# Optimization experiments

Hardware: AMD Instinct MI355X
Metric: run time of the kernel (lower is better)

The kernel has to match this reference:

```python
import jax, jax.numpy as jnp
import numpy as np

EPS = 1e-08
NORMALIZE = True


def setup_inputs() -> dict:
    key = jax.random.key(0)
    X = jax.random.normal(key, (1024, 256), dtype=jnp.float32)
    return {"X": X}


def reference(X):
    # Optional L2 normalization (torch F.normalize: x / max(||x||_2, eps))
    if NORMALIZE:
        norm = jnp.linalg.norm(X, axis=-1, keepdims=True)
        X = X / jnp.maximum(norm, EPS)
    n, d = X.shape
    # Pairwise abs differences: [n, n, d]
    dists = jnp.abs(X[None, :, :] - X[:, None, :])
    # Faithful replication of the original flat-stride diagonal fill:
    # dists.view(-1)[::n+1].fill_(inf) over the flattened n*n*d tensor.
    flat = dists.reshape(-1)
    idx = jnp.arange(0, n * n * d, n + 1)
    flat = flat.at[idx].set(jnp.inf)
    dists = flat.reshape(n, n, d)
    # Min over axis 1 (nearest neighbour per (i, feature)), then -log
    m = jnp.min(dists, axis=1)  # [n, d]
    return -jnp.sum(jnp.log(m + EPS)) / n
```

## Files before the change

kernel.cpp:

```cpp
#include <hip/hip_runtime.h>
#include <math.h>

#define N 1024
#define D 256
#define EPSF 1e-8f
#define K2_BLOCKS 32
#define ROWS_PER_BLK (N / K2_BLOCKS)
#define LANES_PER_ROW (256 / ROWS_PER_BLK)

__global__ void __launch_bounds__(256) rownorm_kernel(const float* __restrict__ X,
                                                      float* __restrict__ y,
                                                      float* __restrict__ accum,
                                                      int* __restrict__ cnt) {
    const int tid  = threadIdx.x;
    const int wave = tid >> 6;
    const int lane = tid & 63;
    const int row  = blockIdx.x * 4 + wave;

    const float4 v = ((const float4*)(X + row * D))[lane];
    float ss = v.x * v.x + v.y * v.y + v.z * v.z + v.w * v.w;
    #pragma unroll
    for (int off = 32; off > 0; off >>= 1)
        ss += __shfl_down(ss, off, 64);

    if (lane == 0) {
        y[row] = v.x / fmaxf(sqrtf(ss), EPSF);
    }
    if (blockIdx.x == 0 && tid == 0) { *accum = 0.0f; *cnt = 0; }
}

__global__ void __launch_bounds__(256) koleo_kernel(const float* __restrict__ y,
                                                    float* __restrict__ accum,
                                                    int* __restrict__ cnt,
                                                    float* __restrict__ out) {
    __shared__ float sy[N];
    const int tid = threadIdx.x;
    ((float4*)sy)[tid] = ((const float4*)y)[tid];
    __syncthreads();

    const int grp = tid >> 3;
    const int s   = tid & 7;
    const int i   = blockIdx.x * ROWS_PER_BLK + grp;
    const float yi = sy[i];

    float m = INFINITY;
    #pragma unroll 8
    for (int t = 0; t < N / LANES_PER_ROW; ++t) {
        const int j = s + (t << 3);
        float d = fabsf(sy[j] - yi);
        d = (j == i) ? INFINITY : d;
        m = fminf(m, d);
    }
    #pragma unroll
    for (int off = 4; off > 0; off >>= 1)
        m = fminf(m, __shfl_xor(m, off, 64));

    float val = (s == 0) ? -logf(m + EPSF) : 0.0f;
    #pragma unroll
    for (int off = 32; off > 0; off >>= 1)
        val += __shfl_down(val, off, 64);

    __shared__ float wsum[4];
    if ((tid & 63) == 0) wsum[tid >> 6] = val;
    __syncthreads();

    if (tid == 0) {
        const float part = wsum[0] + wsum[1] + wsum[2] + wsum[3];
        atomicAdd(accum, part);
        __threadfence();
        const int ticket = atomicAdd(cnt, 1);
        if (ticket == K2_BLOCKS - 1) {
            const float total = atomicAdd(accum, 0.0f);
            out[0] = total * (1.0f / (float)N) - 255.0f * logf(EPSF);
        }
    }
}

extern "C" void kernel_launch(void* const* d_in, const int* in_sizes, int n_in,
                              void* d_out, int out_size, void* d_ws, size_t ws_size,
                              hipStream_t stream) {
    const float* X = (const float*)d_in[0];
    float* out = (float*)d_out;
    float* y     = (float*)d_ws;
    float* accum = (float*)d_ws + N;
    int*   cnt   = (int*)((float*)d_ws + N + 1);

    rownorm_kernel<<<N / 4, 256, 0, stream>>>(X, y, accum, cnt);
    koleo_kernel<<<K2_BLOCKS, 256, 0, stream>>>(y, accum, cnt, out);
}
```

Baseline: 63.47 us.

## Fuse row normalization into the nearest-neighbour kernel with redundant per-block norms

Merges the row-norm kernel and the KoLeo reduction kernel into a single kernel. Each of 16 blocks recomputes the normalized first feature for all 1024 rows into shared memory, then scans with float4 reads. The intermediate workspace buffer and the ticket-counter final reduction are dropped: blocks atomically add pre-scaled partials into an output that a memset clears first. This removes one kernel launch and the cross-block ticket, but every block now reads the whole input redundantly, and the norm phase runs only 16 blocks of parallelism.

```diff
diff --git a/kernel.cpp b/kernel.cpp
--- a/kernel.cpp
+++ b/kernel.cpp
@@ -3,59 +3,67 @@
 
 #define N 1024
 #define D 256
+#define D4 (D / 4)
 #define EPSF 1e-8f
-#define K2_BLOCKS 32
-#define ROWS_PER_BLK (N / K2_BLOCKS)
-#define LANES_PER_ROW (256 / ROWS_PER_BLK)
+#define B 16
+#define RPB (N / B)
 
-__global__ void __launch_bounds__(256) rownorm_kernel(const float* __restrict__ X,
-                                                      float* __restrict__ y,
-                                                      float* __restrict__ accum,
-                                                      int* __restrict__ cnt) {
-    const int tid  = threadIdx.x;
-    const int wave = tid >> 6;
-    const int lane = tid & 63;
-    const int row  = blockIdx.x * 4 + wave;
-
-    const float4 v = ((const float4*)(X + row * D))[lane];
-    float ss = v.x * v.x + v.y * v.y + v.z * v.z + v.w * v.w;
-    #pragma unroll
-    for (int off = 32; off > 0; off >>= 1)
-        ss += __shfl_down(ss, off, 64);
-
-    if (lane == 0) {
-        y[row] = v.x / fmaxf(sqrtf(ss), EPSF);
-    }
-    if (blockIdx.x == 0 && tid == 0) { *accum = 0.0f; *cnt = 0; }
-}
-
-__global__ void __launch_bounds__(256) koleo_kernel(const float* __restrict__ y,
-                                                    float* __restrict__ accum,
-                                                    int* __restrict__ cnt,
-                                                    float* __restrict__ out) {
+__global__ void __launch_bounds__(256) koleo_fused(const float* __restrict__ X,
+                                                   float* __restrict__ out) {
     __shared__ float sy[N];
     const int tid = threadIdx.x;
-    ((float4*)sy)[tid] = ((const float4*)y)[tid];
+
+    {
+        const int g = tid >> 3;
+        const int s = tid & 7;
+        const float4* X4 = (const float4*)X;
+        for (int pass = 0; pass < 32; ++pass) {
+            const int r = pass * 32 + g;
+            const float4* row = X4 + r * D4;
+            float ss = 0.0f;
+            float x0 = 0.0f;
+            #pragma unroll
+            for (int it = 0; it < 8; ++it) {
+                const float4 v = row[s + (it << 3)];
+                if (it == 0) x0 = v.x;
+                ss += v.x * v.x + v.y * v.y + v.z * v.z + v.w * v.w;
+            }
+            #pragma unroll
+            for (int off = 4; off > 0; off >>= 1)
+                ss += __shfl_xor(ss, off, 64);
+            if (s == 0)
+                sy[r] = x0 / fmaxf(sqrtf(ss), EPSF);
+        }
+    }
     __syncthreads();
 
-    const int grp = tid >> 3;
-    const int s   = tid & 7;
-    const int i   = blockIdx.x * ROWS_PER_BLK + grp;
+    const int grp = tid >> 2;
+    const int s   = tid & 3;
+    const int i   = blockIdx.x * RPB + grp;
     const float yi = sy[i];
+    const float4* sy4 = (const float4*)sy;
 
     float m = INFINITY;
     #pragma unroll 8
-    for (int t = 0; t < N / LANES_PER_ROW; ++t) {
-        const int j = s + (t << 3);
-        float d = fabsf(sy[j] - yi);
-        d = (j == i) ? INFINITY : d;
-        m = fminf(m, d);
+    for (int t = 0; t < 64; ++t) {
+        const int q  = s + (t << 2);
+        const float4 v = sy4[q];
+        const int jb = q << 2;
+        float d0 = fabsf(v.x - yi);
+        float d1 = fabsf(v.y - yi);
+        float d2 = fabsf(v.z - yi);
+        float d3 = fabsf(v.w - yi);
+        d0 = (jb + 0 == i) ? INFINITY : d0;
+        d1 = (jb + 1 == i) ? INFINITY : d1;
+        d2 = (jb + 2 == i) ? INFINITY : d2;
+        d3 = (jb + 3 == i) ? INFINITY : d3;
+        m = fminf(m, fminf(fminf(d0, d1), fminf(d2, d3)));
     }
     #pragma unroll
-    for (int off = 4; off > 0; off >>= 1)
+    for (int off = 2; off > 0; off >>= 1)
         m = fminf(m, __shfl_xor(m, off, 64));
 
-    float val = (s == 0) ? -logf(m + EPSF) : 0.0f;
+    float val = (s == 0) ? (-logf(m + EPSF) * (1.0f / (float)N)) : 0.0f;
     #pragma unroll
     for (int off = 32; off > 0; off >>= 1)
         val += __shfl_down(val, off, 64);
@@ -65,26 +73,15 @@
     __syncthreads();
 
     if (tid == 0) {
-        const float part = wsum[0] + wsum[1] + wsum[2] + wsum[3];
-        atomicAdd(accum, part);
-        __threadfence();
-        const int ticket = atomicAdd(cnt, 1);
-        if (ticket == K2_BLOCKS - 1) {
-            const float total = atomicAdd(accum, 0.0f);
-            out[0] = total * (1.0f / (float)N) - 255.0f * logf(EPSF);
-        }
+        float part = wsum[0] + wsum[1] + wsum[2] + wsum[3];
+        if (blockIdx.x == 0) part += -255.0f * logf(EPSF);
+        atomicAdd(out, part);
     }
 }
 
 extern "C" void kernel_launch(void* const* d_in, const int* in_sizes, int n_in,
                               void* d_out, int out_size, void* d_ws, size_t ws_size,
                               hipStream_t stream) {
-    const float* X = (const float*)d_in[0];
-    float* out = (float*)d_out;
-    float* y     = (float*)d_ws;
-    float* accum = (float*)d_ws + N;
-    int*   cnt   = (int*)((float*)d_ws + N + 1);
-
-    rownorm_kernel<<<N / 4, 256, 0, stream>>>(X, y, accum, cnt);
-    koleo_kernel<<<K2_BLOCKS, 256, 0, stream>>>(y, accum, cnt, out);
+    hipMemsetAsync(d_out, 0, out_size, stream);
+    koleo_fused<<<B, 256, 0, stream>>>((const float*)d_in[0], (float*)d_out);
 }
```

After: 78.90 us. 24.3% more time.

## Spread nearest-neighbour scan over more blocks and accumulate directly into output

Applied to the files above, without the earlier changes.

The second kernel now runs 128 blocks of 8 rows each, with 32 lanes per row reading shared memory as float4, instead of 32 blocks with 8 lanes per row reading scalars. The ticket-counter epilogue is removed. The first kernel writes the constant term into the output, and each block atomically adds its pre-scaled partial sum straight into it. This is meant to shorten the serial per-thread loop and remove the fence and second atomic. In exchange it does four times as many global atomics, and the result now depends on the first kernel having initialised the output.

```diff
diff --git a/kernel.cpp b/kernel.cpp
--- a/kernel.cpp
+++ b/kernel.cpp
@@ -4,14 +4,11 @@
 #define N 1024
 #define D 256
 #define EPSF 1e-8f
-#define K2_BLOCKS 32
-#define ROWS_PER_BLK (N / K2_BLOCKS)
-#define LANES_PER_ROW (256 / ROWS_PER_BLK)
+#define K2_BLOCKS 128
 
 __global__ void __launch_bounds__(256) rownorm_kernel(const float* __restrict__ X,
                                                       float* __restrict__ y,
-                                                      float* __restrict__ accum,
-                                                      int* __restrict__ cnt) {
+                                                      float* __restrict__ out) {
     const int tid  = threadIdx.x;
     const int wave = tid >> 6;
     const int lane = tid & 63;
@@ -26,36 +23,44 @@
     if (lane == 0) {
         y[row] = v.x / fmaxf(sqrtf(ss), EPSF);
     }
-    if (blockIdx.x == 0 && tid == 0) { *accum = 0.0f; *cnt = 0; }
+    if (blockIdx.x == 0 && tid == 0)
+        out[0] = -255.0f * logf(EPSF);
 }
 
 __global__ void __launch_bounds__(256) koleo_kernel(const float* __restrict__ y,
-                                                    float* __restrict__ accum,
-                                                    int* __restrict__ cnt,
                                                     float* __restrict__ out) {
     __shared__ float sy[N];
     const int tid = threadIdx.x;
     ((float4*)sy)[tid] = ((const float4*)y)[tid];
     __syncthreads();
 
-    const int grp = tid >> 3;
-    const int s   = tid & 7;
-    const int i   = blockIdx.x * ROWS_PER_BLK + grp;
+    const int grp = tid >> 5;
+    const int s   = tid & 31;
+    const int i   = blockIdx.x * 8 + grp;
     const float yi = sy[i];
+    const float4* sy4 = (const float4*)sy;
 
     float m = INFINITY;
-    #pragma unroll 8
-    for (int t = 0; t < N / LANES_PER_ROW; ++t) {
-        const int j = s + (t << 3);
-        float d = fabsf(sy[j] - yi);
-        d = (j == i) ? INFINITY : d;
-        m = fminf(m, d);
+    #pragma unroll
+    for (int t = 0; t < 8; ++t) {
+        const int q  = s + (t << 5);
+        const float4 v = sy4[q];
+        const int jb = q << 2;
+        float d0 = fabsf(v.x - yi);
+        float d1 = fabsf(v.y - yi);
+        float d2 = fabsf(v.z - yi);
+        float d3 = fabsf(v.w - yi);
+        d0 = (jb + 0 == i) ? INFINITY : d0;
+        d1 = (jb + 1 == i) ? INFINITY : d1;
+        d2 = (jb + 2 == i) ? INFINITY : d2;
+        d3 = (jb + 3 == i) ? INFINITY : d3;
+        m = fminf(m, fminf(fminf(d0, d1), fminf(d2, d3)));
     }
     #pragma unroll
-    for (int off = 4; off > 0; off >>= 1)
+    for (int off = 16; off > 0; off >>= 1)
         m = fminf(m, __shfl_xor(m, off, 64));
 
-    float val = (s == 0) ? -logf(m + EPSF) : 0.0f;
+    float val = (s == 0) ? (-logf(m + EPSF) * (1.0f / (float)N)) : 0.0f;
     #pragma unroll
     for (int off = 32; off > 0; off >>= 1)
         val += __shfl_down(val, off, 64);
@@ -66,13 +71,7 @@
 
     if (tid == 0) {
         const float part = wsum[0] + wsum[1] + wsum[2] + wsum[3];
-        atomicAdd(accum, part);
-        __threadfence();
-        const int ticket = atomicAdd(cnt, 1);
-        if (ticket == K2_BLOCKS - 1) {
-            const float total = atomicAdd(accum, 0.0f);
-            out[0] = total * (1.0f / (float)N) - 255.0f * logf(EPSF);
-        }
+        atomicAdd(out, part);
     }
 }
 
@@ -81,10 +80,8 @@
                               hipStream_t stream) {
     const float* X = (const float*)d_in[0];
     float* out = (float*)d_out;
-    float* y     = (float*)d_ws;
-    float* accum = (float*)d_ws + N;
-    int*   cnt   = (int*)((float*)d_ws + N + 1);
+    float* y   = (float*)d_ws;
 
-    rownorm_kernel<<<N / 4, 256, 0, stream>>>(X, y, accum, cnt);
-    koleo_kernel<<<K2_BLOCKS, 256, 0, stream>>>(y, accum, cnt, out);
+    rownorm_kernel<<<N / 4, 256, 0, stream>>>(X, y, out);
+    koleo_kernel<<<K2_BLOCKS, 256, 0, stream>>>(y, out);
 }
```

New measurement: 56.21 us (median of 2 runs). 11.4% less time.
